# Optimization experiments

Measured on AMD Instinct MI355X. Metric: run time of the kernel, lower is better.

Reference implementation:

```python
import jax, jax.numpy as jnp
import numpy as np

DIM = 1024
KEY = 128
UV = 1024  # dim * mlp_ratio // 2
SCALE = 1.0 / np.sqrt(KEY).astype(np.float32)
NEG_INF = 1e12


def _sinusoidal(n, d):
    # RoPE tables: sin/cos of shape [n, d//2]
    pos = np.arange(n)[:, None].astype(np.float32)
    inv = (1.0 / 10000 ** (np.arange(0, d, 2).astype(np.float32) / d))[None, :]
    ang = pos * inv
    return jnp.asarray(np.sin(ang)), jnp.asarray(np.cos(ang))


def setup_inputs() -> dict:
    key = jax.random.key(0)
    ks = jax.random.split(key, 4)
    B, N = 4, 2048
    hidden_states = jax.random.normal(ks[0], (B, N, DIM), dtype=jnp.float32)
    attention_mask = jax.random.randint(ks[1], (B, N, N), 0, 2).astype(jnp.int32)
    sin, cos = _sinusoidal(N, KEY)
    Wi = jax.random.normal(ks[2], (DIM, UV * 2 + KEY), dtype=jnp.float32) * (DIM ** -0.5)
    bi = jnp.zeros((UV * 2 + KEY,), jnp.float32)
    Wo = jax.random.normal(ks[3], (UV, DIM), dtype=jnp.float32) * (UV ** -0.5)
    bo = jnp.zeros((DIM,), jnp.float32)
    return {
        "hidden_states": hidden_states, "attention_mask": attention_mask,
        "sin": sin, "cos": cos, "Wi": Wi, "bi": bi, "Wo": Wo, "bo": bo,
        "q_gamma": jnp.ones((KEY,), jnp.float32), "q_beta": jnp.zeros((KEY,), jnp.float32),
        "k_gamma": jnp.ones((KEY,), jnp.float32), "k_beta": jnp.zeros((KEY,), jnp.float32),
    }


def _rotary(x, sin, cos):
    # x: [b, n, d]; sin/cos: [n, d//2]; interleaved RoPE, concat layout
    x1, x2 = x[..., 0::2], x[..., 1::2]
    return jnp.concatenate([x1 * cos - x2 * sin, x1 * sin + x2 * cos], axis=-1)


def reference(hidden_states, attention_mask, sin, cos, Wi, bi, Wo, bo,
              q_gamma, q_beta, k_gamma, k_beta):
    x = jax.nn.silu(hidden_states @ Wi + bi)            # [b, n, 2176]
    u, v, qk = x[..., :UV], x[..., UV:2 * UV], x[..., 2 * UV:]
    q = _rotary(qk * q_gamma + q_beta, sin, cos)        # [b, n, 128]
    k = _rotary(qk * k_gamma + k_beta, sin, cos)
    a = jnp.einsum('bmd,bnd->bmn', q, k) * SCALE        # [b, m, n]
    mask = attention_mask != 0
    a = jnp.where(mask, a, -NEG_INF)
    ll = attention_mask.sum(-1, keepdims=True).astype(a.dtype)  # [b, m, 1]
    A = jnp.square(jax.nn.relu(a)) / ll                 # squared_relu normalize
    out = (u * jnp.einsum('bmn,bnd->bmd', A, v)) @ Wo + bo
    return out
```

## Files before the change

kernel.cpp:

```cpp
#include <hip/hip_runtime.h>
#include <hip/hip_bf16.h>
#include <cstdint>

#define DIM   1024
#define KEY   128
#define UV    1024
#define NCOL  (UV*2 + KEY)
#define SEQ   2048
#define BATCH 4
#define MTOT  (BATCH*SEQ)
#define SCALE 0.08838834764831845f

typedef __attribute__((ext_vector_type(8))) short short8;
typedef __attribute__((ext_vector_type(4))) float f32x4;

__device__ inline unsigned short f2b(float x) {
  unsigned int u = __float_as_uint(x);
  unsigned int r = (u + 0x7fffu + ((u >> 16) & 1u)) >> 16;
  return (unsigned short)r;
}
__device__ inline float b2f(unsigned short x) {
  return __uint_as_float(((unsigned int)x) << 16);
}

__device__ inline void gload_lds16(const void* g, void* l) {
  __builtin_amdgcn_global_load_lds(
      (const __attribute__((address_space(1))) unsigned int*)g,
      (__attribute__((address_space(3))) unsigned int*)l, 16, 0, 0);
}

__device__ __forceinline__ void gemm8w_256x128(
    const unsigned short* __restrict__ A, int lda,
    const unsigned short* __restrict__ Bt, int ldb,
    int K, f32x4 acc[4][4], unsigned short* lds) {
  const int tid  = threadIdx.x;
  const int lane = tid & 63;
  const int wid  = tid >> 6;
  const int wm   = wid >> 1;
  const int wn   = wid & 1;
  const int fr   = lane & 15;
  const int fq   = lane >> 4;

  unsigned short* ldsA = lds;
  unsigned short* ldsB = lds + 3 * 16384;

#pragma unroll
  for (int i = 0; i < 4; ++i)
#pragma unroll
    for (int j = 0; j < 4; ++j) acc[i][j] = (f32x4){0.f, 0.f, 0.f, 0.f};

  auto stage = [&](int t, int b) {
    const unsigned short* Ag = A + (size_t)t * 64;
    const unsigned short* Bg = Bt + (size_t)t * 64;
    unsigned short* la = ldsA + b * 16384;
    unsigned short* lb = ldsB + b * 8192;
#pragma unroll
    for (int p = 0; p < 4; ++p) {
      int c = p * 512 + tid, r = c >> 3, q = c & 7;
      int qs = q ^ (r & 7);
      gload_lds16(Ag + (size_t)r * lda + qs * 8, la + ((size_t)(p * 512 + wid * 64)) * 8);
    }
#pragma unroll
    for (int p = 0; p < 2; ++p) {
      int c = p * 512 + tid, r = c >> 3, q = c & 7;
      int qs = q ^ (r & 7);
      gload_lds16(Bg + (size_t)r * ldb + qs * 8, lb + ((size_t)(p * 512 + wid * 64)) * 8);
    }
  };

  const int colk0 = ((fq ^ (fr & 7)) * 8);
  const int rA    = (wm * 64 + fr) * 64;
  const int rB    = (wn * 64 + fr) * 64;

  const int NT = K >> 6;
  stage(0, 0);
  stage(1, 1);
  asm volatile("s_waitcnt vmcnt(6)" ::: "memory");
  __builtin_amdgcn_s_barrier();
  asm volatile("" ::: "memory");

  int cur = 0;
  for (int t = 0; t < NT; ++t) {
    unsigned short* la = ldsA + cur * 16384;
    unsigned short* lb = ldsB + cur * 8192;
    const int c2 = (cur >= 1) ? cur - 1 : 2;
    const bool more = (t + 2) < NT;
    if (more) stage(t + 2, c2);

    short8 af[4], bf[4];
#pragma unroll
    for (int i = 0; i < 4; ++i) af[i] = *(const short8*)&la[rA + i * 1024 + colk0];
#pragma unroll
    for (int j = 0; j < 4; ++j) bf[j] = *(const short8*)&lb[rB + j * 1024 + colk0];
    __builtin_amdgcn_s_barrier();
    asm volatile("" ::: "memory");
    __builtin_amdgcn_s_setprio(1);
#pragma unroll
    for (int i = 0; i < 4; ++i)
#pragma unroll
      for (int j = 0; j < 4; ++j)
        acc[i][j] = __builtin_amdgcn_mfma_f32_16x16x32_bf16(af[i], bf[j], acc[i][j], 0, 0, 0);
    __builtin_amdgcn_s_setprio(0);
#pragma unroll
    for (int i = 0; i < 4; ++i) af[i] = *(const short8*)&la[rA + i * 1024 + (colk0 ^ 32)];
#pragma unroll
    for (int j = 0; j < 4; ++j) bf[j] = *(const short8*)&lb[rB + j * 1024 + (colk0 ^ 32)];
    __builtin_amdgcn_s_barrier();
    asm volatile("" ::: "memory");
    __builtin_amdgcn_s_setprio(1);
#pragma unroll
    for (int i = 0; i < 4; ++i)
#pragma unroll
      for (int j = 0; j < 4; ++j)
        acc[i][j] = __builtin_amdgcn_mfma_f32_16x16x32_bf16(af[i], bf[j], acc[i][j], 0, 0, 0);
    __builtin_amdgcn_s_setprio(0);
    asm volatile("" ::: "memory");
    if (more) asm volatile("s_waitcnt vmcnt(6)" ::: "memory");
    else      asm volatile("s_waitcnt vmcnt(0)" ::: "memory");
    __builtin_amdgcn_s_barrier();
    asm volatile("" ::: "memory");
    cur = (cur == 2) ? 0 : cur + 1;
  }
}

#define EPILOGUE_COORDS()                      \
  const int lane = threadIdx.x & 63;           \
  const int wid  = threadIdx.x >> 6;           \
  const int wm   = wid >> 1, wn = wid & 1;     \
  const int fr   = lane & 15;                  \
  const int fq   = lane >> 4;

__global__ __launch_bounds__(256) void k_cvt(const float* __restrict__ in,
                                             unsigned short* __restrict__ out) {
  int id = blockIdx.x * 256 + threadIdx.x;
  float4 f = ((const float4*)in)[id];
  ushort4 o;
  o.x = f2b(f.x); o.y = f2b(f.y); o.z = f2b(f.z); o.w = f2b(f.w);
  ((ushort4*)out)[id] = o;
}

__global__ void k_tcvt(const float* __restrict__ in, unsigned short* __restrict__ out,
                       int R, int C) {
  __shared__ float t[32][33];
  int c0 = blockIdx.x * 32, r0 = blockIdx.y * 32;
  int tx = threadIdx.x, ty = threadIdx.y;
#pragma unroll
  for (int i = 0; i < 4; ++i)
    t[ty + i * 8][tx] = in[(size_t)(r0 + ty + i * 8) * C + c0 + tx];
  __syncthreads();
#pragma unroll
  for (int i = 0; i < 4; ++i)
    out[(size_t)(c0 + ty + i * 8) * R + r0 + tx] = f2b(t[tx][ty + i * 8]);
}

__global__ __launch_bounds__(256) void k_masksum(const int* __restrict__ mask,
                                                 float* __restrict__ ll) {
  int wid = threadIdx.x >> 6, lane = threadIdx.x & 63;
  int row = blockIdx.x * 4 + wid;
  const int4* p = (const int4*)(mask + (size_t)row * SEQ);
  int s = 0;
#pragma unroll
  for (int i = 0; i < 8; ++i) { int4 v = p[lane + 64 * i]; s += v.x + v.y + v.z + v.w; }
  for (int off = 32; off; off >>= 1) s += __shfl_down(s, off);
  if (lane == 0) ll[row] = (float)s;
}

__global__ __launch_bounds__(256) void k_rope(const float* __restrict__ qk,
                                              const float* __restrict__ sn,
                                              const float* __restrict__ cs,
                                              const float* __restrict__ qg,
                                              const float* __restrict__ qb,
                                              const float* __restrict__ kg,
                                              const float* __restrict__ kb,
                                              unsigned short* __restrict__ q,
                                              unsigned short* __restrict__ k) {
  int id = blockIdx.x * 256 + threadIdx.x;
  int m = id >> 6, t = id & 63;
  int n = m & (SEQ - 1);
  float x1 = qk[m * KEY + 2 * t], x2 = qk[m * KEY + 2 * t + 1];
  float s_ = sn[n * 64 + t], c_ = cs[n * 64 + t];
  float a1 = x1 * qg[2 * t] + qb[2 * t];
  float a2 = x2 * qg[2 * t + 1] + qb[2 * t + 1];
  q[m * KEY + t]      = f2b(a1 * c_ - a2 * s_);
  q[m * KEY + 64 + t] = f2b(a1 * s_ + a2 * c_);
  float b1 = x1 * kg[2 * t] + kb[2 * t];
  float b2 = x2 * kg[2 * t + 1] + kb[2 * t + 1];
  k[m * KEY + t]      = f2b(b1 * c_ - b2 * s_);
  k[m * KEY + 64 + t] = f2b(b1 * s_ + b2 * c_);
}

__global__ __launch_bounds__(256) void k_vT(const unsigned short* __restrict__ v,
                                            unsigned short* __restrict__ vT) {
  __shared__ unsigned short t[64][65];
  int b = blockIdx.z;
  int n0 = blockIdx.x * 64;
  int d0 = blockIdx.y * 64;
  int tid = threadIdx.x;
  int r = tid >> 4;
  int c4 = (tid & 15) * 4;
#pragma unroll
  for (int i = 0; i < 4; ++i) {
    int n = n0 + r + i * 16;
    ushort4 val = *(const ushort4*)&v[((size_t)b * SEQ + n) * UV + d0 + c4];
    t[c4 + 0][r + i * 16] = val.x;
    t[c4 + 1][r + i * 16] = val.y;
    t[c4 + 2][r + i * 16] = val.z;
    t[c4 + 3][r + i * 16] = val.w;
  }
  __syncthreads();
#pragma unroll
  for (int i = 0; i < 4; ++i) {
    int d = d0 + r + i * 16;
    ushort4 o;
    o.x = t[r + i * 16][c4 + 0];
    o.y = t[r + i * 16][c4 + 1];
    o.z = t[r + i * 16][c4 + 2];
    o.w = t[r + i * 16][c4 + 3];
    *(ushort4*)&vT[((size_t)b * UV + d) * SEQ + n0 + c4] = o;
  }
}

#define LDS_BYTES 147456

__global__ __launch_bounds__(512, 2) void k_gemm1(const unsigned short* __restrict__ hbf,
                                                  const unsigned short* __restrict__ WiT,
                                                  const float* __restrict__ bi,
                                                  unsigned short* __restrict__ u,
                                                  unsigned short* __restrict__ v,
                                                  float* __restrict__ qk) {
  extern __shared__ unsigned short lds[];
  int m0 = blockIdx.x * 256, n0 = blockIdx.y * 128;
  f32x4 acc[4][4];
  gemm8w_256x128(hbf + (size_t)m0 * DIM, DIM, WiT + (size_t)n0 * DIM, DIM, DIM, acc, lds);
  EPILOGUE_COORDS();
#pragma unroll
  for (int i = 0; i < 4; ++i)
#pragma unroll
    for (int j = 0; j < 4; ++j)
#pragma unroll
      for (int r = 0; r < 4; ++r) {
        int row = m0 + wm * 64 + i * 16 + fq * 4 + r;
        int col = n0 + wn * 64 + j * 16 + fr;
        float x = acc[i][j][r] + bi[col];
        float s = x / (1.f + __expf(-x));
        if (n0 < UV)            u[(size_t)row * UV + col] = f2b(s);
        else if (n0 < 2 * UV)   v[(size_t)row * UV + col - UV] = f2b(s);
        else                    qk[(size_t)row * KEY + col - 2 * UV] = s;
      }
}

__global__ __launch_bounds__(512, 2) void k_qk(const unsigned short* __restrict__ q,
                                               const unsigned short* __restrict__ k,
                                               const int* __restrict__ mask,
                                               const float* __restrict__ ll,
                                               unsigned short* __restrict__ Abuf) {
  extern __shared__ unsigned short lds[];
  int b = blockIdx.z;
  int m0 = blockIdx.x * 256, n0 = blockIdx.y * 128;
  f32x4 acc[4][4];
  gemm8w_256x128(q + ((size_t)b * SEQ + m0) * KEY, KEY,
                 k + ((size_t)b * SEQ + n0) * KEY, KEY, KEY, acc, lds);
  EPILOGUE_COORDS();
#pragma unroll
  for (int i = 0; i < 4; ++i)
#pragma unroll
    for (int j = 0; j < 4; ++j)
#pragma unroll
      for (int r = 0; r < 4; ++r) {
        int row = m0 + wm * 64 + i * 16 + fq * 4 + r;
        int col = n0 + wn * 64 + j * 16 + fr;
        float a = acc[i][j][r] * SCALE;
        int mk = mask[((size_t)b * SEQ + row) * SEQ + col];
        float rel = (mk != 0 && a > 0.f) ? a : 0.f;
        float Av = rel * rel / ll[b * SEQ + row];
        Abuf[((size_t)b * SEQ + row) * SEQ + col] = f2b(Av);
      }
}

__global__ __launch_bounds__(512, 2) void k_av(const unsigned short* __restrict__ Abuf,
                                               const unsigned short* __restrict__ vT,
                                               const unsigned short* __restrict__ u,
                                               unsigned short* __restrict__ g) {
  extern __shared__ unsigned short lds[];
  int b = blockIdx.z;
  int m0 = blockIdx.x * 256, n0 = blockIdx.y * 128;
  f32x4 acc[4][4];
  gemm8w_256x128(Abuf + ((size_t)b * SEQ + m0) * SEQ, SEQ,
                 vT + ((size_t)b * UV + n0) * SEQ, SEQ, SEQ, acc, lds);
  EPILOGUE_COORDS();
#pragma unroll
  for (int i = 0; i < 4; ++i)
#pragma unroll
    for (int j = 0; j < 4; ++j)
#pragma unroll
      for (int r = 0; r < 4; ++r) {
        int row = m0 + wm * 64 + i * 16 + fq * 4 + r;
        int col = n0 + wn * 64 + j * 16 + fr;
        size_t gi = ((size_t)b * SEQ + row) * UV + col;
        g[gi] = f2b(acc[i][j][r] * b2f(u[gi]));
      }
}

__global__ __launch_bounds__(512, 2) void k_out(const unsigned short* __restrict__ g,
                                                const unsigned short* __restrict__ WoT,
                                                const float* __restrict__ bo,
                                                float* __restrict__ out) {
  extern __shared__ unsigned short lds[];
  int m0 = blockIdx.x * 256, n0 = blockIdx.y * 128;
  f32x4 acc[4][4];
  gemm8w_256x128(g + (size_t)m0 * UV, UV, WoT + (size_t)n0 * UV, UV, UV, acc, lds);
  EPILOGUE_COORDS();
#pragma unroll
  for (int i = 0; i < 4; ++i)
#pragma unroll
    for (int j = 0; j < 4; ++j)
#pragma unroll
      for (int r = 0; r < 4; ++r) {
        int row = m0 + wm * 64 + i * 16 + fq * 4 + r;
        int col = n0 + wn * 64 + j * 16 + fr;
        out[(size_t)row * DIM + col] = acc[i][j][r] + bo[col];
      }
}

extern "C" void kernel_launch(void* const* d_in, const int* in_sizes, int n_in,
                              void* d_out, int out_size, void* d_ws, size_t ws_size,
                              hipStream_t stream) {
  const float* h    = (const float*)d_in[0];
  const int*   mask = (const int*)d_in[1];
  const float* sn   = (const float*)d_in[2];
  const float* cs   = (const float*)d_in[3];
  const float* Wi   = (const float*)d_in[4];
  const float* bi   = (const float*)d_in[5];
  const float* Wo   = (const float*)d_in[6];
  const float* bo   = (const float*)d_in[7];
  const float* qg   = (const float*)d_in[8];
  const float* qb   = (const float*)d_in[9];
  const float* kg   = (const float*)d_in[10];
  const float* kb   = (const float*)d_in[11];
  float* out = (float*)d_out;

  static_assert(LDS_BYTES == (3 * 16384 + 3 * 8192) * 2, "lds size");
  hipFuncSetAttribute((const void*)k_gemm1, hipFuncAttributeMaxDynamicSharedMemorySize, LDS_BYTES);
  hipFuncSetAttribute((const void*)k_qk,    hipFuncAttributeMaxDynamicSharedMemorySize, LDS_BYTES);
  hipFuncSetAttribute((const void*)k_av,    hipFuncAttributeMaxDynamicSharedMemorySize, LDS_BYTES);
  hipFuncSetAttribute((const void*)k_out,   hipFuncAttributeMaxDynamicSharedMemorySize, LDS_BYTES);

  char* ws = (char*)d_ws;
  size_t off = 0;
  auto alloc = [&](size_t bytes) { void* p = ws + off; off += (bytes + 255) & ~(size_t)255; return p; };
  unsigned short* hbf  = (unsigned short*)alloc((size_t)MTOT * DIM * 2);
  unsigned short* WiT  = (unsigned short*)alloc((size_t)NCOL * DIM * 2);
  unsigned short* WoT  = (unsigned short*)alloc((size_t)DIM * UV * 2);
  unsigned short* u    = (unsigned short*)alloc((size_t)MTOT * UV * 2);
  unsigned short* v    = (unsigned short*)alloc((size_t)MTOT * UV * 2);
  unsigned short* vT   = (unsigned short*)alloc((size_t)MTOT * UV * 2);
  float*          qkb  = (float*)alloc((size_t)MTOT * KEY * 4);
  unsigned short* qbuf = (unsigned short*)alloc((size_t)MTOT * KEY * 2);
  unsigned short* kbuf = (unsigned short*)alloc((size_t)MTOT * KEY * 2);
  float*          ll   = (float*)alloc((size_t)MTOT * 4);
  unsigned short* Abuf = (unsigned short*)alloc((size_t)BATCH * SEQ * SEQ * 2);
  unsigned short* g    = (unsigned short*)alloc((size_t)MTOT * UV * 2);

  k_cvt<<<(MTOT * DIM / 4) / 256, 256, 0, stream>>>(h, hbf);
  k_tcvt<<<dim3(NCOL / 32, DIM / 32), dim3(32, 8), 0, stream>>>(Wi, WiT, DIM, NCOL);
  k_tcvt<<<dim3(UV / 32, DIM / 32), dim3(32, 8), 0, stream>>>(Wo, WoT, DIM, UV);
  k_masksum<<<MTOT / 4, 256, 0, stream>>>(mask, ll);

  k_gemm1<<<dim3(MTOT / 256, NCOL / 128), 512, LDS_BYTES, stream>>>(hbf, WiT, bi, u, v, qkb);
  k_rope<<<(MTOT * 64) / 256, 256, 0, stream>>>(qkb, sn, cs, qg, qb, kg, kb, qbuf, kbuf);
  k_vT<<<dim3(SEQ / 64, UV / 64, BATCH), 256, 0, stream>>>(v, vT);
  k_qk<<<dim3(SEQ / 256, SEQ / 128, BATCH), 512, LDS_BYTES, stream>>>(qbuf, kbuf, mask, ll, Abuf);
  k_av<<<dim3(SEQ / 256, UV / 128, BATCH), 512, LDS_BYTES, stream>>>(Abuf, vT, u, g);
  k_out<<<dim3(MTOT / 256, DIM / 128), 512, LDS_BYTES, stream>>>(g, WoT, bo, out);
}
```

Before: 205.1 us.

## Restructure GEMM pipeline into 4-phase half-K stages, swizzle blocks across XCDs, bit-pack mask

```diff
diff --git a/kernel.cpp b/kernel.cpp
--- a/kernel.cpp
+++ b/kernel.cpp
@@ -29,7 +29,9 @@
       (__attribute__((address_space(3))) unsigned int*)l, 16, 0, 0);
 }
 
-__device__ __forceinline__ void gemm8w_256x128(
+#define BARX() do { asm volatile("" ::: "memory"); __builtin_amdgcn_s_barrier(); asm volatile("" ::: "memory"); } while (0)
+
+__device__ __forceinline__ void gemm4ph(
     const unsigned short* __restrict__ A, int lda,
     const unsigned short* __restrict__ Bt, int ldb,
     int K, f32x4 acc[4][4], unsigned short* lds) {
@@ -42,85 +44,74 @@
   const int fq   = lane >> 4;
 
   unsigned short* ldsA = lds;
-  unsigned short* ldsB = lds + 3 * 16384;
+  unsigned short* ldsB = lds + 32768;
 
 #pragma unroll
   for (int i = 0; i < 4; ++i)
 #pragma unroll
     for (int j = 0; j < 4; ++j) acc[i][j] = (f32x4){0.f, 0.f, 0.f, 0.f};
 
-  auto stage = [&](int t, int b) {
-    const unsigned short* Ag = A + (size_t)t * 64;
-    const unsigned short* Bg = Bt + (size_t)t * 64;
-    unsigned short* la = ldsA + b * 16384;
-    unsigned short* lb = ldsB + b * 8192;
-#pragma unroll
-    for (int p = 0; p < 4; ++p) {
-      int c = p * 512 + tid, r = c >> 3, q = c & 7;
-      int qs = q ^ (r & 7);
-      gload_lds16(Ag + (size_t)r * lda + qs * 8, la + ((size_t)(p * 512 + wid * 64)) * 8);
-    }
+  auto stA = [&](int t, int d, int h) {
+    const unsigned short* g = A + (size_t)t * 64 + h * 32;
+    unsigned short* l = ldsA + d * 16384 + h * 8192;
 #pragma unroll
     for (int p = 0; p < 2; ++p) {
-      int c = p * 512 + tid, r = c >> 3, q = c & 7;
-      int qs = q ^ (r & 7);
-      gload_lds16(Bg + (size_t)r * ldb + qs * 8, lb + ((size_t)(p * 512 + wid * 64)) * 8);
+      int c = p * 512 + tid;
+      gload_lds16(g + (size_t)(c >> 2) * lda + (c & 3) * 8,
+                  l + (size_t)(p * 512 + wid * 64) * 8);
     }
   };
-
-  const int colk0 = ((fq ^ (fr & 7)) * 8);
-  const int rA    = (wm * 64 + fr) * 64;
-  const int rB    = (wn * 64 + fr) * 64;
+  auto stB = [&](int t, int d, int h) {
+    const unsigned short* g = Bt + (size_t)t * 64 + h * 32;
+    unsigned short* l = ldsB + d * 8192 + h * 4096;
+    gload_lds16(g + (size_t)(tid >> 2) * ldb + (tid & 3) * 8,
+                l + (size_t)(wid * 64) * 8);
+  };
+
+  const int aoff = (wm * 64 + fr) * 32 + fq * 8;
+  const int boff = (wn * 64 + fr) * 32 + fq * 8;
+
+#define LDAB(d, h)                                                            \
+  _Pragma("unroll") for (int i = 0; i < 4; ++i) {                             \
+    af[i] = *(const short8*)&ldsA[(d) * 16384 + (h) * 8192 + aoff + i * 512]; \
+    bf[i] = *(const short8*)&ldsB[(d) * 8192 + (h) * 4096 + boff + i * 512];  \
+  }
+#define MFMA16()                                                              \
+  __builtin_amdgcn_s_setprio(1);                                              \
+  _Pragma("unroll") for (int i = 0; i < 4; ++i)                               \
+  _Pragma("unroll") for (int j = 0; j < 4; ++j)                               \
+    acc[i][j] = __builtin_amdgcn_mfma_f32_16x16x32_bf16(af[i], bf[j], acc[i][j], 0, 0, 0); \
+  __builtin_amdgcn_s_setprio(0);
 
   const int NT = K >> 6;
-  stage(0, 0);
-  stage(1, 1);
-  asm volatile("s_waitcnt vmcnt(6)" ::: "memory");
-  __builtin_amdgcn_s_barrier();
-  asm volatile("" ::: "memory");
-
-  int cur = 0;
-  for (int t = 0; t < NT; ++t) {
-    unsigned short* la = ldsA + cur * 16384;
-    unsigned short* lb = ldsB + cur * 8192;
-    const int c2 = (cur >= 1) ? cur - 1 : 2;
-    const bool more = (t + 2) < NT;
-    if (more) stage(t + 2, c2);
-
+  const int NI = NT >> 1;
+
+  stA(0, 0, 0); stB(0, 0, 0);
+  stA(0, 0, 1); stB(0, 0, 1);
+  stA(1, 1, 0); stB(1, 1, 0);
+  asm volatile("s_waitcnt vmcnt(3)" ::: "memory");
+  BARX();
+
+  auto ktp = [&](int T, bool more) {
     short8 af[4], bf[4];
-#pragma unroll
-    for (int i = 0; i < 4; ++i) af[i] = *(const short8*)&la[rA + i * 1024 + colk0];
-#pragma unroll
-    for (int j = 0; j < 4; ++j) bf[j] = *(const short8*)&lb[rB + j * 1024 + colk0];
-    __builtin_amdgcn_s_barrier();
-    asm volatile("" ::: "memory");
-    __builtin_amdgcn_s_setprio(1);
-#pragma unroll
-    for (int i = 0; i < 4; ++i)
-#pragma unroll
-      for (int j = 0; j < 4; ++j)
-        acc[i][j] = __builtin_amdgcn_mfma_f32_16x16x32_bf16(af[i], bf[j], acc[i][j], 0, 0, 0);
-    __builtin_amdgcn_s_setprio(0);
-#pragma unroll
-    for (int i = 0; i < 4; ++i) af[i] = *(const short8*)&la[rA + i * 1024 + (colk0 ^ 32)];
-#pragma unroll
-    for (int j = 0; j < 4; ++j) bf[j] = *(const short8*)&lb[rB + j * 1024 + (colk0 ^ 32)];
-    __builtin_amdgcn_s_barrier();
-    asm volatile("" ::: "memory");
-    __builtin_amdgcn_s_setprio(1);
-#pragma unroll
-    for (int i = 0; i < 4; ++i)
-#pragma unroll
-      for (int j = 0; j < 4; ++j)
-        acc[i][j] = __builtin_amdgcn_mfma_f32_16x16x32_bf16(af[i], bf[j], acc[i][j], 0, 0, 0);
-    __builtin_amdgcn_s_setprio(0);
-    asm volatile("" ::: "memory");
-    if (more) asm volatile("s_waitcnt vmcnt(6)" ::: "memory");
+    LDAB(0, 0); stA(T + 1, 1, 1); stB(T + 1, 1, 1);
+    BARX(); MFMA16(); BARX();
+    LDAB(0, 1); if (more) { stA(T + 2, 0, 0); stB(T + 2, 0, 0); }
+    BARX(); MFMA16();
+    if (more) asm volatile("s_waitcnt vmcnt(3)" ::: "memory");
     else      asm volatile("s_waitcnt vmcnt(0)" ::: "memory");
-    __builtin_amdgcn_s_barrier();
-    asm volatile("" ::: "memory");
-    cur = (cur == 2) ? 0 : cur + 1;
-  }
+    BARX();
+    LDAB(1, 0); if (more) { stA(T + 2, 0, 1); stB(T + 2, 0, 1); }
+    BARX(); MFMA16(); BARX();
+    LDAB(1, 1); if (more) { stA(T + 3, 1, 0); stB(T + 3, 1, 0); }
+    BARX(); MFMA16();
+    if (more) asm volatile("s_waitcnt vmcnt(3)" ::: "memory");
+    BARX();
+  };
+  for (int i = 0; i + 1 < NI; ++i) ktp(2 * i, true);
+  ktp(2 * (NI - 1), false);
+#undef LDAB
+#undef MFMA16
 }
 
 #define EPILOGUE_COORDS()                      \
@@ -129,6 +120,15 @@
   const int wm   = wid >> 1, wn = wid & 1;     \
   const int fr   = lane & 15;                  \
   const int fq   = lane >> 4;
+
+__device__ __forceinline__ void xcd_swz(int& tx, int& ty) {
+  const int gx = gridDim.x, gy = gridDim.y;
+  const int n = gx * gy;
+  const int D = blockIdx.y * gx + blockIdx.x;
+  const int c = (D & 7) * (n >> 3) + (D >> 3);
+  tx = c / gy;
+  ty = c - tx * gy;
+}
 
 __global__ __launch_bounds__(256) void k_cvt(const float* __restrict__ in,
                                              unsigned short* __restrict__ out) {
@@ -153,14 +153,25 @@
     out[(size_t)(c0 + ty + i * 8) * R + r0 + tx] = f2b(t[tx][ty + i * 8]);
 }
 
-__global__ __launch_bounds__(256) void k_masksum(const int* __restrict__ mask,
-                                                 float* __restrict__ ll) {
+__global__ __launch_bounds__(256) void k_maskprep(const int* __restrict__ mask,
+                                                  float* __restrict__ ll,
+                                                  unsigned int* __restrict__ mb) {
   int wid = threadIdx.x >> 6, lane = threadIdx.x & 63;
   int row = blockIdx.x * 4 + wid;
   const int4* p = (const int4*)(mask + (size_t)row * SEQ);
   int s = 0;
 #pragma unroll
-  for (int i = 0; i < 8; ++i) { int4 v = p[lane + 64 * i]; s += v.x + v.y + v.z + v.w; }
+  for (int i = 0; i < 8; ++i) {
+    int4 v = p[i * 64 + lane];
+    unsigned nib = (v.x != 0 ? 1u : 0u) | (v.y != 0 ? 2u : 0u) |
+                   (v.z != 0 ? 4u : 0u) | (v.w != 0 ? 8u : 0u);
+    unsigned w = 0;
+#pragma unroll
+    for (int k2 = 0; k2 < 8; ++k2)
+      w |= __shfl(nib, (lane & ~7) + k2, 64) << (4 * k2);
+    if ((lane & 7) == 0) mb[(size_t)row * 64 + i * 8 + (lane >> 3)] = w;
+    s += v.x + v.y + v.z + v.w;
+  }
   for (int off = 32; off; off >>= 1) s += __shfl_down(s, off);
   if (lane == 0) ll[row] = (float)s;
 }
@@ -220,7 +231,7 @@
   }
 }
 
-#define LDS_BYTES 147456
+#define LDS_BYTES 98304
 
 __global__ __launch_bounds__(512, 2) void k_gemm1(const unsigned short* __restrict__ hbf,
                                                   const unsigned short* __restrict__ WiT,
@@ -229,9 +240,10 @@
                                                   unsigned short* __restrict__ v,
                                                   float* __restrict__ qk) {
   extern __shared__ unsigned short lds[];
-  int m0 = blockIdx.x * 256, n0 = blockIdx.y * 128;
+  int tx, ty; xcd_swz(tx, ty);
+  int m0 = tx * 256, n0 = ty * 128;
   f32x4 acc[4][4];
-  gemm8w_256x128(hbf + (size_t)m0 * DIM, DIM, WiT + (size_t)n0 * DIM, DIM, DIM, acc, lds);
+  gemm4ph(hbf + (size_t)m0 * DIM, DIM, WiT + (size_t)n0 * DIM, DIM, DIM, acc, lds);
   EPILOGUE_COORDS();
 #pragma unroll
   for (int i = 0; i < 4; ++i)
@@ -251,30 +263,35 @@
 
 __global__ __launch_bounds__(512, 2) void k_qk(const unsigned short* __restrict__ q,
                                                const unsigned short* __restrict__ k,
-                                               const int* __restrict__ mask,
+                                               const unsigned int* __restrict__ mb,
                                                const float* __restrict__ ll,
                                                unsigned short* __restrict__ Abuf) {
   extern __shared__ unsigned short lds[];
   int b = blockIdx.z;
-  int m0 = blockIdx.x * 256, n0 = blockIdx.y * 128;
+  int tx, ty; xcd_swz(tx, ty);
+  int m0 = tx * 256, n0 = ty * 128;
   f32x4 acc[4][4];
-  gemm8w_256x128(q + ((size_t)b * SEQ + m0) * KEY, KEY,
-                 k + ((size_t)b * SEQ + n0) * KEY, KEY, KEY, acc, lds);
+  gemm4ph(q + ((size_t)b * SEQ + m0) * KEY, KEY,
+          k + ((size_t)b * SEQ + n0) * KEY, KEY, KEY, acc, lds);
   EPILOGUE_COORDS();
 #pragma unroll
   for (int i = 0; i < 4; ++i)
 #pragma unroll
-    for (int j = 0; j < 4; ++j)
-#pragma unroll
-      for (int r = 0; r < 4; ++r) {
-        int row = m0 + wm * 64 + i * 16 + fq * 4 + r;
+    for (int r = 0; r < 4; ++r) {
+      int row = m0 + wm * 64 + i * 16 + fq * 4 + r;
+      size_t rb = (size_t)b * SEQ + row;
+      unsigned long long mw =
+          *(const unsigned long long*)&mb[rb * 64 + (n0 >> 5) + wn * 2];
+      float rll = 1.0f / ll[rb];
+#pragma unroll
+      for (int j = 0; j < 4; ++j) {
         int col = n0 + wn * 64 + j * 16 + fr;
         float a = acc[i][j][r] * SCALE;
-        int mk = mask[((size_t)b * SEQ + row) * SEQ + col];
-        float rel = (mk != 0 && a > 0.f) ? a : 0.f;
-        float Av = rel * rel / ll[b * SEQ + row];
-        Abuf[((size_t)b * SEQ + row) * SEQ + col] = f2b(Av);
+        bool on = (mw >> (j * 16 + fr)) & 1ull;
+        float rel = (on && a > 0.f) ? a : 0.f;
+        Abuf[rb * SEQ + col] = f2b(rel * rel * rll);
       }
+    }
 }
 
 __global__ __launch_bounds__(512, 2) void k_av(const unsigned short* __restrict__ Abuf,
@@ -283,10 +300,11 @@
                                                unsigned short* __restrict__ g) {
   extern __shared__ unsigned short lds[];
   int b = blockIdx.z;
-  int m0 = blockIdx.x * 256, n0 = blockIdx.y * 128;
+  int tx, ty; xcd_swz(tx, ty);
+  int m0 = tx * 256, n0 = ty * 128;
   f32x4 acc[4][4];
-  gemm8w_256x128(Abuf + ((size_t)b * SEQ + m0) * SEQ, SEQ,
-                 vT + ((size_t)b * UV + n0) * SEQ, SEQ, SEQ, acc, lds);
+  gemm4ph(Abuf + ((size_t)b * SEQ + m0) * SEQ, SEQ,
+          vT + ((size_t)b * UV + n0) * SEQ, SEQ, SEQ, acc, lds);
   EPILOGUE_COORDS();
 #pragma unroll
   for (int i = 0; i < 4; ++i)
@@ -306,9 +324,10 @@
                                                 const float* __restrict__ bo,
                                                 float* __restrict__ out) {
   extern __shared__ unsigned short lds[];
-  int m0 = blockIdx.x * 256, n0 = blockIdx.y * 128;
+  int tx, ty; xcd_swz(tx, ty);
+  int m0 = tx * 256, n0 = ty * 128;
   f32x4 acc[4][4];
-  gemm8w_256x128(g + (size_t)m0 * UV, UV, WoT + (size_t)n0 * UV, UV, UV, acc, lds);
+  gemm4ph(g + (size_t)m0 * UV, UV, WoT + (size_t)n0 * UV, UV, UV, acc, lds);
   EPILOGUE_COORDS();
 #pragma unroll
   for (int i = 0; i < 4; ++i)
@@ -339,7 +358,6 @@
   const float* kb   = (const float*)d_in[11];
   float* out = (float*)d_out;
 
-  static_assert(LDS_BYTES == (3 * 16384 + 3 * 8192) * 2, "lds size");
   hipFuncSetAttribute((const void*)k_gemm1, hipFuncAttributeMaxDynamicSharedMemorySize, LDS_BYTES);
   hipFuncSetAttribute((const void*)k_qk,    hipFuncAttributeMaxDynamicSharedMemorySize, LDS_BYTES);
   hipFuncSetAttribute((const void*)k_av,    hipFuncAttributeMaxDynamicSharedMemorySize, LDS_BYTES);
@@ -358,18 +376,19 @@
   unsigned short* qbuf = (unsigned short*)alloc((size_t)MTOT * KEY * 2);
   unsigned short* kbuf = (unsigned short*)alloc((size_t)MTOT * KEY * 2);
   float*          ll   = (float*)alloc((size_t)MTOT * 4);
+  unsigned int*   mbits= (unsigned int*)alloc((size_t)MTOT * 64 * 4);
   unsigned short* Abuf = (unsigned short*)alloc((size_t)BATCH * SEQ * SEQ * 2);
   unsigned short* g    = (unsigned short*)alloc((size_t)MTOT * UV * 2);
 
   k_cvt<<<(MTOT * DIM / 4) / 256, 256, 0, stream>>>(h, hbf);
   k_tcvt<<<dim3(NCOL / 32, DIM / 32), dim3(32, 8), 0, stream>>>(Wi, WiT, DIM, NCOL);
   k_tcvt<<<dim3(UV / 32, DIM / 32), dim3(32, 8), 0, stream>>>(Wo, WoT, DIM, UV);
-  k_masksum<<<MTOT / 4, 256, 0, stream>>>(mask, ll);
+  k_maskprep<<<MTOT / 4, 256, 0, stream>>>(mask, ll, mbits);
 
   k_gemm1<<<dim3(MTOT / 256, NCOL / 128), 512, LDS_BYTES, stream>>>(hbf, WiT, bi, u, v, qkb);
   k_rope<<<(MTOT * 64) / 256, 256, 0, stream>>>(qkb, sn, cs, qg, qb, kg, kb, qbuf, kbuf);
   k_vT<<<dim3(SEQ / 64, UV / 64, BATCH), 256, 0, stream>>>(v, vT);
-  k_qk<<<dim3(SEQ / 256, SEQ / 128, BATCH), 512, LDS_BYTES, stream>>>(qbuf, kbuf, mask, ll, Abuf);
+  k_qk<<<dim3(SEQ / 256, SEQ / 128, BATCH), 512, LDS_BYTES, stream>>>(qbuf, kbuf, mbits, ll, Abuf);
   k_av<<<dim3(SEQ / 256, UV / 128, BATCH), 512, LDS_BYTES, stream>>>(Abuf, vT, u, g);
   k_out<<<dim3(MTOT / 256, DIM / 128), 512, LDS_BYTES, stream>>>(g, WoT, bo, out);
 }
```

Measured after the change: 204.4 us. About the same (-0.3%).
